# Kernel tuning notes

Measured on AMD Instinct MI355X. Metric: run time of the kernel, lower is better.

Reference implementation:

```python
import jax, jax.numpy as jnp
import numpy as np

B, T, N_EMBD, HEAD = 8, 2048, 1024, 64


def setup_inputs() -> dict:
    key = jax.random.key(0)
    kx, kq, kk, kv = jax.random.split(key, 4)
    s = 1.0 / np.sqrt(N_EMBD)
    return {
        "x": jax.random.normal(kx, (B, T, N_EMBD), dtype=jnp.float32),
        "Wq": jax.random.normal(kq, (N_EMBD, HEAD), dtype=jnp.float32) * s,
        "Wk": jax.random.normal(kk, (N_EMBD, HEAD), dtype=jnp.float32) * s,
        "Wv": jax.random.normal(kv, (N_EMBD, HEAD), dtype=jnp.float32) * s,
    }


def reference(x, Wq, Wk, Wv):
    # x: [B, T, C] with C = n_embd
    Bs, Ts, C = x.shape
    q = jnp.einsum('btc,ch->bth', x, Wq)  # [B,T,H]
    k = jnp.einsum('btc,ch->bth', x, Wk)
    v = jnp.einsum('btc,ch->bth', x, Wv)
    # NOTE: original scales by C**-0.5 where C = n_embd (input dim), not head_size
    scale = jnp.asarray(C, x.dtype) ** -0.5
    wei = jnp.einsum('bth,bsh->bts', q, k) * scale  # [B,T,T]
    causal = jnp.tril(jnp.ones((Ts, Ts), dtype=bool))
    wei = jnp.where(causal, wei, jnp.asarray(-jnp.inf, wei.dtype))
    wei = jax.nn.softmax(wei, axis=-1)
    out = jnp.einsum('bts,bsh->bth', wei, v)  # [B,T,H]
    return out
```

## Files before the change

kernel.cpp:

```cpp
#include <hip/hip_runtime.h>
#include <hip/hip_bf16.h>
#include <math.h>

#define B_ 8
#define T_ 2048
#define C_ 1024
#define H_ 64

typedef __attribute__((ext_vector_type(8))) __bf16 bf16x8;
typedef __attribute__((ext_vector_type(4))) float f32x4;

static __device__ inline unsigned short f2bf_u(float f) {
    __bf16 b = (__bf16)f;
    return __builtin_bit_cast(unsigned short, b);
}
static __device__ inline unsigned int pack2(float lo, float hi) {
    return (unsigned int)f2bf_u(lo) | ((unsigned int)f2bf_u(hi) << 16);
}

__global__ void prep_w_kernel(const float* __restrict__ Wq,
                              const float* __restrict__ Wk,
                              const float* __restrict__ Wv,
                              unsigned short* __restrict__ Wp) {
    int idx = blockIdx.x * 256 + threadIdx.x;
    if (idx >= C_ * 192) return;
    int k = idx / 192;
    int n = idx % 192;
    const float* W = (n < 64) ? Wq : (n < 128) ? Wk : Wv;
    float val = W[k * 64 + (n & 63)];
    Wp[((size_t)(k >> 5) * 192 + n) * 32 + (k & 31)] = f2bf_u(val);
}

__global__ __launch_bounds__(256, 3) void proj_kernel(
        const float* __restrict__ x, const unsigned short* __restrict__ Wp,
        unsigned short* __restrict__ q, unsigned short* __restrict__ k,
        unsigned short* __restrict__ vT) {
    __shared__ f32x4 red[4][12][64];
    const int wave = threadIdx.x >> 6;
    const int lane = threadIdx.x & 63;
    const int col  = lane & 15;
    const int quad = lane >> 4;
    const int row0 = blockIdx.x * 16;
    const float* xrow = x + (size_t)(row0 + col) * C_ + quad * 8;

    f32x4 acc[12];
    #pragma unroll
    for (int i = 0; i < 12; i++) acc[i] = (f32x4){0.f, 0.f, 0.f, 0.f};

    const int kt0 = wave * 8;
    #pragma unroll 4
    for (int kt = kt0; kt < kt0 + 8; kt++) {
        const float4* xp = (const float4*)(xrow + kt * 32);
        float4 x0 = xp[0];
        float4 x1 = xp[1];
        bf16x8 a;
        a[0] = (__bf16)x0.x; a[1] = (__bf16)x0.y; a[2] = (__bf16)x0.z; a[3] = (__bf16)x0.w;
        a[4] = (__bf16)x1.x; a[5] = (__bf16)x1.y; a[6] = (__bf16)x1.z; a[7] = (__bf16)x1.w;
        const unsigned short* wb = Wp + ((size_t)kt * 192 + col) * 32 + quad * 8;
        #pragma unroll
        for (int n = 0; n < 12; n++) {
            bf16x8 bfrag = *(const bf16x8*)(wb + n * (16 * 32));
            acc[n] = __builtin_amdgcn_mfma_f32_16x16x32_bf16(a, bfrag, acc[n], 0, 0, 0);
        }
    }
    #pragma unroll
    for (int n = 0; n < 12; n++) red[wave][n][lane] = acc[n];
    __syncthreads();

    const int bi   = row0 >> 11;
    const int trow = row0 & 2047;
    #pragma unroll
    for (int j = 0; j < 3; j++) {
        int n = wave * 3 + j;
        f32x4 s = red[0][n][lane];
        s += red[1][n][lane];
        s += red[2][n][lane];
        s += red[3][n][lane];
        if (n < 8) {
            unsigned short* dst = (n < 4) ? q : k;
            int cc = (n & 3) * 16 + col;
            #pragma unroll
            for (int r = 0; r < 4; r++) {
                int grow = row0 + quad * 4 + r;
                dst[(size_t)grow * 64 + cc] = f2bf_u(s[r]);
            }
        } else {
            int hh = (n - 8) * 16 + col;
            ushort4 pk;
            pk.x = f2bf_u(s[0]); pk.y = f2bf_u(s[1]);
            pk.z = f2bf_u(s[2]); pk.w = f2bf_u(s[3]);
            *(ushort4*)(vT + ((size_t)bi * 64 + hh) * T_ + trow + quad * 4) = pk;
        }
    }
}

__global__ __launch_bounds__(256, 4) void attn_kernel(
        const unsigned short* __restrict__ q, const unsigned short* __restrict__ k,
        const unsigned short* __restrict__ vT, float* __restrict__ out) {
    __shared__ unsigned int tbuf[4][2][16 * 20];
    __shared__ float so[4][16][68];
    __shared__ float sl[4][16];
    const int wave = threadIdx.x >> 6;
    const int lane = threadIdx.x & 63;
    const int col  = lane & 15;
    const int quad = lane >> 4;
    const int bi = blockIdx.x & 7;
    const int ti = 127 - (blockIdx.x >> 3);
    const int t0 = ti * 16;
    const unsigned short* qb = q  + (size_t)bi * T_ * 64;
    const unsigned short* kb = k  + (size_t)bi * T_ * 64;
    const unsigned short* vb = vT + (size_t)bi * 64 * T_;

    bf16x8 qf0 = *(const bf16x8*)(qb + (size_t)(t0 + col) * 64 + quad * 8);
    bf16x8 qf1 = *(const bf16x8*)(qb + (size_t)(t0 + col) * 64 + 32 + quad * 8);

    f32x4 o[4];
    #pragma unroll
    for (int i = 0; i < 4; i++) o[i] = (f32x4){0.f, 0.f, 0.f, 0.f};
    float lacc = 0.f;
    const float cs = 0.03125f * 1.44269504088896f;
    const int qrow = t0 + col;

    const int nit = (t0 + 47) >> 5;
    const int ci  = (nit + 3) >> 2;
    const int it0 = wave * ci;
    const int it1 = min(it0 + ci, nit);

    for (int it = it0; it < it1; ++it) {
        const int s0 = it * 32;
        bf16x8 kf00 = *(const bf16x8*)(kb + (size_t)(s0 + col) * 64 + quad * 8);
        bf16x8 kf01 = *(const bf16x8*)(kb + (size_t)(s0 + col) * 64 + 32 + quad * 8);
        bf16x8 kf10 = *(const bf16x8*)(kb + (size_t)(s0 + 16 + col) * 64 + quad * 8);
        bf16x8 kf11 = *(const bf16x8*)(kb + (size_t)(s0 + 16 + col) * 64 + 32 + quad * 8);
        f32x4 sa = (f32x4){0.f, 0.f, 0.f, 0.f};
        f32x4 sb = (f32x4){0.f, 0.f, 0.f, 0.f};
        sa = __builtin_amdgcn_mfma_f32_16x16x32_bf16(kf00, qf0, sa, 0, 0, 0);
        sa = __builtin_amdgcn_mfma_f32_16x16x32_bf16(kf01, qf1, sa, 0, 0, 0);
        sb = __builtin_amdgcn_mfma_f32_16x16x32_bf16(kf10, qf0, sb, 0, 0, 0);
        sb = __builtin_amdgcn_mfma_f32_16x16x32_bf16(kf11, qf1, sb, 0, 0, 0);

        float pa[4], pb[4];
        #pragma unroll
        for (int r = 0; r < 4; r++) {
            int ka = s0 + quad * 4 + r;
            pa[r] = (ka      <= qrow) ? exp2f(sa[r] * cs) : 0.f;
            pb[r] = (ka + 16 <= qrow) ? exp2f(sb[r] * cs) : 0.f;
            lacc += pa[r] + pb[r];
        }
        unsigned int* tb = &tbuf[wave][it & 1][0];
        *(uint2*)&tb[col * 20 + 2 * quad] =
            make_uint2(pack2(pa[0], pa[1]), pack2(pa[2], pa[3]));
        *(uint2*)&tb[col * 20 + 8 + 2 * quad] =
            make_uint2(pack2(pb[0], pb[1]), pack2(pb[2], pb[3]));
        bf16x8 pf = *(const bf16x8*)&tb[col * 20 + 4 * quad];
        #pragma unroll
        for (int ht = 0; ht < 4; ht++) {
            bf16x8 vf = *(const bf16x8*)(vb + (size_t)(ht * 16 + col) * T_ + s0 + quad * 8);
            o[ht] = __builtin_amdgcn_mfma_f32_16x16x32_bf16(vf, pf, o[ht], 0, 0, 0);
        }
    }

    lacc += __shfl_xor(lacc, 16);
    lacc += __shfl_xor(lacc, 32);
    if (quad == 0) sl[wave][col] = lacc;
    #pragma unroll
    for (int ht = 0; ht < 4; ht++)
        *(f32x4*)&so[wave][col][ht * 16 + quad * 4] = o[ht];
    __syncthreads();

    for (int e = threadIdx.x; e < 1024; e += 256) {
        int qq = e >> 6, h = e & 63;
        float L = sl[0][qq] + sl[1][qq] + sl[2][qq] + sl[3][qq];
        float val = so[0][qq][h] + so[1][qq][h] + so[2][qq][h] + so[3][qq][h];
        out[((size_t)bi * T_ + t0 + qq) * 64 + h] = val / L;
    }
}

extern "C" void kernel_launch(void* const* d_in, const int* in_sizes, int n_in,
                              void* d_out, int out_size, void* d_ws, size_t ws_size,
                              hipStream_t stream) {
    const float* x  = (const float*)d_in[0];
    const float* Wq = (const float*)d_in[1];
    const float* Wk = (const float*)d_in[2];
    const float* Wv = (const float*)d_in[3];
    float* out = (float*)d_out;

    unsigned short* Wp  = (unsigned short*)d_ws;
    unsigned short* qws = (unsigned short*)((char*)d_ws + 0x60000);
    unsigned short* kws = (unsigned short*)((char*)d_ws + 0x60000 + 0x200000);
    unsigned short* vws = (unsigned short*)((char*)d_ws + 0x60000 + 0x400000);

    prep_w_kernel<<<(C_ * 192 + 255) / 256, 256, 0, stream>>>(Wq, Wk, Wv, Wp);
    proj_kernel<<<(B_ * T_) / 16, 256, 0, stream>>>(x, Wp, qws, kws, vws);
    attn_kernel<<<(B_ * T_) / 16, 256, 0, stream>>>(qws, kws, vws, out);
}
```

Before: 160.3 us.

## Restructure projection kernel to stage weight slice in LDS and split outputs across blocks

The projection kernel now launches 192 blocks of 512 threads. Each block takes one 64-column slice of the packed weights (Q, K or V) and loads all of it into shared memory with global_load_lds. Each wave then computes a full-K 32x64 output tile, so the cross-wave reduction through shared memory goes away. In exchange, x is read three times (once per projection group), and only 192 blocks are launched, which may underfill the GPU.

```diff
diff --git a/kernel.cpp b/kernel.cpp
--- a/kernel.cpp
+++ b/kernel.cpp
@@ -31,65 +31,89 @@
     Wp[((size_t)(k >> 5) * 192 + n) * 32 + (k & 31)] = f2bf_u(val);
 }
 
-__global__ __launch_bounds__(256, 3) void proj_kernel(
+__global__ __launch_bounds__(512) void proj_kernel(
         const float* __restrict__ x, const unsigned short* __restrict__ Wp,
         unsigned short* __restrict__ q, unsigned short* __restrict__ k,
         unsigned short* __restrict__ vT) {
-    __shared__ f32x4 red[4][12][64];
+    __shared__ unsigned short wlds[32][64][32];
     const int wave = threadIdx.x >> 6;
     const int lane = threadIdx.x & 63;
     const int col  = lane & 15;
     const int quad = lane >> 4;
-    const int row0 = blockIdx.x * 16;
-    const float* xrow = x + (size_t)(row0 + col) * C_ + quad * 8;
-
-    f32x4 acc[12];
-    #pragma unroll
-    for (int i = 0; i < 12; i++) acc[i] = (f32x4){0.f, 0.f, 0.f, 0.f};
-
-    const int kt0 = wave * 8;
+    const int g     = blockIdx.x % 3;
+    const int chunk = blockIdx.x / 3;
+    const int n0 = g * 64;
+
+    #pragma unroll
+    for (int i = 0; i < 4; i++) {
+        int kt = wave * 4 + i;
+        #pragma unroll
+        for (int part = 0; part < 4; part++) {
+            const unsigned short* src =
+                Wp + ((size_t)kt * 192 + n0 + part * 16) * 32 + lane * 8;
+            __builtin_amdgcn_global_load_lds(
+                (const __attribute__((address_space(1))) unsigned int*)src,
+                (__attribute__((address_space(3))) unsigned int*)&wlds[kt][part * 16][0],
+                16, 0, 0);
+        }
+    }
+    __syncthreads();
+
+    const int r0 = chunk * 256 + wave * 32;
+    const float* xb0 = x + (size_t)(r0 + col) * C_;
+    const float* xb1 = x + (size_t)(r0 + 16 + col) * C_;
+
+    f32x4 acc[8];
+    #pragma unroll
+    for (int i = 0; i < 8; i++) acc[i] = (f32x4){0.f, 0.f, 0.f, 0.f};
+
     #pragma unroll 4
-    for (int kt = kt0; kt < kt0 + 8; kt++) {
-        const float4* xp = (const float4*)(xrow + kt * 32);
-        float4 x0 = xp[0];
-        float4 x1 = xp[1];
-        bf16x8 a;
-        a[0] = (__bf16)x0.x; a[1] = (__bf16)x0.y; a[2] = (__bf16)x0.z; a[3] = (__bf16)x0.w;
-        a[4] = (__bf16)x1.x; a[5] = (__bf16)x1.y; a[6] = (__bf16)x1.z; a[7] = (__bf16)x1.w;
-        const unsigned short* wb = Wp + ((size_t)kt * 192 + col) * 32 + quad * 8;
-        #pragma unroll
-        for (int n = 0; n < 12; n++) {
-            bf16x8 bfrag = *(const bf16x8*)(wb + n * (16 * 32));
-            acc[n] = __builtin_amdgcn_mfma_f32_16x16x32_bf16(a, bfrag, acc[n], 0, 0, 0);
-        }
-    }
-    #pragma unroll
-    for (int n = 0; n < 12; n++) red[wave][n][lane] = acc[n];
-    __syncthreads();
-
-    const int bi   = row0 >> 11;
-    const int trow = row0 & 2047;
-    #pragma unroll
-    for (int j = 0; j < 3; j++) {
-        int n = wave * 3 + j;
-        f32x4 s = red[0][n][lane];
-        s += red[1][n][lane];
-        s += red[2][n][lane];
-        s += red[3][n][lane];
-        if (n < 8) {
-            unsigned short* dst = (n < 4) ? q : k;
-            int cc = (n & 3) * 16 + col;
+    for (int kt = 0; kt < 32; kt++) {
+        const float4* xq0 = (const float4*)(xb0 + kt * 32 + quad * 8);
+        const float4* xq1 = (const float4*)(xb1 + kt * 32 + quad * 8);
+        float4 p00 = xq0[0], p01 = xq0[1];
+        float4 p10 = xq1[0], p11 = xq1[1];
+        bf16x8 a0, a1;
+        a0[0] = (__bf16)p00.x; a0[1] = (__bf16)p00.y; a0[2] = (__bf16)p00.z; a0[3] = (__bf16)p00.w;
+        a0[4] = (__bf16)p01.x; a0[5] = (__bf16)p01.y; a0[6] = (__bf16)p01.z; a0[7] = (__bf16)p01.w;
+        a1[0] = (__bf16)p10.x; a1[1] = (__bf16)p10.y; a1[2] = (__bf16)p10.z; a1[3] = (__bf16)p10.w;
+        a1[4] = (__bf16)p11.x; a1[5] = (__bf16)p11.y; a1[6] = (__bf16)p11.z; a1[7] = (__bf16)p11.w;
+        #pragma unroll
+        for (int nt = 0; nt < 4; nt++) {
+            bf16x8 b = *(const bf16x8*)&wlds[kt][nt * 16 + col][quad * 8];
+            acc[nt]     = __builtin_amdgcn_mfma_f32_16x16x32_bf16(a0, b, acc[nt], 0, 0, 0);
+            acc[4 + nt] = __builtin_amdgcn_mfma_f32_16x16x32_bf16(a1, b, acc[4 + nt], 0, 0, 0);
+        }
+    }
+
+    if (g < 2) {
+        unsigned short* dst = (g == 0) ? q : k;
+        #pragma unroll
+        for (int mt = 0; mt < 2; mt++) {
             #pragma unroll
-            for (int r = 0; r < 4; r++) {
-                int grow = row0 + quad * 4 + r;
-                dst[(size_t)grow * 64 + cc] = f2bf_u(s[r]);
+            for (int nt = 0; nt < 4; nt++) {
+                f32x4 s = acc[mt * 4 + nt];
+                int cc = nt * 16 + col;
+                int grow = r0 + mt * 16 + quad * 4;
+                #pragma unroll
+                for (int r = 0; r < 4; r++)
+                    dst[(size_t)(grow + r) * 64 + cc] = f2bf_u(s[r]);
             }
-        } else {
-            int hh = (n - 8) * 16 + col;
-            ushort4 pk;
-            pk.x = f2bf_u(s[0]); pk.y = f2bf_u(s[1]);
-            pk.z = f2bf_u(s[2]); pk.w = f2bf_u(s[3]);
-            *(ushort4*)(vT + ((size_t)bi * 64 + hh) * T_ + trow + quad * 4) = pk;
+        }
+    } else {
+        #pragma unroll
+        for (int mt = 0; mt < 2; mt++) {
+            #pragma unroll
+            for (int nt = 0; nt < 4; nt++) {
+                f32x4 s = acc[mt * 4 + nt];
+                int hh = nt * 16 + col;
+                int row = r0 + mt * 16 + quad * 4;
+                int bi = row >> 11, trow = row & 2047;
+                ushort4 pk;
+                pk.x = f2bf_u(s[0]); pk.y = f2bf_u(s[1]);
+                pk.z = f2bf_u(s[2]); pk.w = f2bf_u(s[3]);
+                *(ushort4*)(vT + ((size_t)bi * 64 + hh) * T_ + trow) = pk;
+            }
         }
     }
 }
@@ -191,6 +215,6 @@
     unsigned short* vws = (unsigned short*)((char*)d_ws + 0x60000 + 0x400000);
 
     prep_w_kernel<<<(C_ * 192 + 255) / 256, 256, 0, stream>>>(Wq, Wk, Wv, Wp);
-    proj_kernel<<<(B_ * T_) / 16, 256, 0, stream>>>(x, Wp, qws, kws, vws);
+    proj_kernel<<<64 * 3, 512, 0, stream>>>(x, Wp, qws, kws, vws);
     attn_kernel<<<(B_ * T_) / 16, 256, 0, stream>>>(qws, kws, vws, out);
 }
```

Measured after the change: 171.5 us. 7.0% more time.

## Split projection N across waves with shared-memory x staging and prefetch

Applied to the files above, without the earlier changes.

The projection kernel no longer splits the K dimension across waves with a shared-memory reduction. Each wave now owns 48 output columns and walks the full K range. The x tile is converted to bf16 once into a triple-buffered shared buffer, with loads rotated among the waves, and W fragments are software-prefetched one step ahead. This removes the cross-wave reduction and the fourfold redundant x loading and conversion, and raises occupancy to 4 blocks per SM. In exchange it adds a __syncthreads on each of the 32 K steps and makes the K loop serial per wave.

```diff
diff --git a/kernel.cpp b/kernel.cpp
--- a/kernel.cpp
+++ b/kernel.cpp
@@ -31,65 +31,89 @@
     Wp[((size_t)(k >> 5) * 192 + n) * 32 + (k & 31)] = f2bf_u(val);
 }
 
-__global__ __launch_bounds__(256, 3) void proj_kernel(
+#define XPAD 40
+__global__ __launch_bounds__(256, 4) void proj_kernel(
         const float* __restrict__ x, const unsigned short* __restrict__ Wp,
         unsigned short* __restrict__ q, unsigned short* __restrict__ k,
         unsigned short* __restrict__ vT) {
-    __shared__ f32x4 red[4][12][64];
+    __shared__ unsigned short xbf[3][16][XPAD];
     const int wave = threadIdx.x >> 6;
     const int lane = threadIdx.x & 63;
     const int col  = lane & 15;
     const int quad = lane >> 4;
     const int row0 = blockIdx.x * 16;
-    const float* xrow = x + (size_t)(row0 + col) * C_ + quad * 8;
-
-    f32x4 acc[12];
-    #pragma unroll
-    for (int i = 0; i < 12; i++) acc[i] = (f32x4){0.f, 0.f, 0.f, 0.f};
-
-    const int kt0 = wave * 8;
-    #pragma unroll 4
-    for (int kt = kt0; kt < kt0 + 8; kt++) {
-        const float4* xp = (const float4*)(xrow + kt * 32);
-        float4 x0 = xp[0];
-        float4 x1 = xp[1];
-        bf16x8 a;
-        a[0] = (__bf16)x0.x; a[1] = (__bf16)x0.y; a[2] = (__bf16)x0.z; a[3] = (__bf16)x0.w;
-        a[4] = (__bf16)x1.x; a[5] = (__bf16)x1.y; a[6] = (__bf16)x1.z; a[7] = (__bf16)x1.w;
-        const unsigned short* wb = Wp + ((size_t)kt * 192 + col) * 32 + quad * 8;
-        #pragma unroll
-        for (int n = 0; n < 12; n++) {
-            bf16x8 bfrag = *(const bf16x8*)(wb + n * (16 * 32));
-            acc[n] = __builtin_amdgcn_mfma_f32_16x16x32_bf16(a, bfrag, acc[n], 0, 0, 0);
-        }
-    }
-    #pragma unroll
-    for (int n = 0; n < 12; n++) red[wave][n][lane] = acc[n];
+    const int n0   = wave * 48;
+
+    const int srow = lane >> 2;
+    const int scol = (lane & 3) * 8;
+    const float* sbase = x + (size_t)(row0 + srow) * C_ + scol;
+
+    f32x4 acc[3];
+    #pragma unroll
+    for (int i = 0; i < 3; i++) acc[i] = (f32x4){0.f, 0.f, 0.f, 0.f};
+
+    if (wave < 2) {
+        const float4* p = (const float4*)(sbase + wave * 32);
+        float4 u0 = p[0], u1 = p[1];
+        bf16x8 w;
+        w[0] = (__bf16)u0.x; w[1] = (__bf16)u0.y; w[2] = (__bf16)u0.z; w[3] = (__bf16)u0.w;
+        w[4] = (__bf16)u1.x; w[5] = (__bf16)u1.y; w[6] = (__bf16)u1.z; w[7] = (__bf16)u1.w;
+        *(bf16x8*)&xbf[wave][srow][scol] = w;
+    }
+    const unsigned short* wb = Wp + (size_t)(n0 + col) * 32 + quad * 8;
+    bf16x8 bcur0 = *(const bf16x8*)(wb);
+    bf16x8 bcur1 = *(const bf16x8*)(wb + 16 * 32);
+    bf16x8 bcur2 = *(const bf16x8*)(wb + 32 * 32);
     __syncthreads();
 
-    const int bi   = row0 >> 11;
-    const int trow = row0 & 2047;
-    #pragma unroll
-    for (int j = 0; j < 3; j++) {
-        int n = wave * 3 + j;
-        f32x4 s = red[0][n][lane];
-        s += red[1][n][lane];
-        s += red[2][n][lane];
-        s += red[3][n][lane];
-        if (n < 8) {
-            unsigned short* dst = (n < 4) ? q : k;
-            int cc = (n & 3) * 16 + col;
+    #pragma unroll 2
+    for (int kt = 0; kt < 32; kt++) {
+        const bool own = (kt + 2 < 32) && (((kt + 2) & 3) == wave);
+        float4 u0, u1;
+        if (own) {
+            const float4* p = (const float4*)(sbase + (kt + 2) * 32);
+            u0 = p[0]; u1 = p[1];
+        }
+        bf16x8 bn0, bn1, bn2;
+        if (kt + 1 < 32) {
+            const unsigned short* wn = wb + (size_t)(kt + 1) * 192 * 32;
+            bn0 = *(const bf16x8*)(wn);
+            bn1 = *(const bf16x8*)(wn + 16 * 32);
+            bn2 = *(const bf16x8*)(wn + 32 * 32);
+        }
+        bf16x8 a = *(const bf16x8*)&xbf[kt % 3][col][quad * 8];
+        acc[0] = __builtin_amdgcn_mfma_f32_16x16x32_bf16(a, bcur0, acc[0], 0, 0, 0);
+        acc[1] = __builtin_amdgcn_mfma_f32_16x16x32_bf16(a, bcur1, acc[1], 0, 0, 0);
+        acc[2] = __builtin_amdgcn_mfma_f32_16x16x32_bf16(a, bcur2, acc[2], 0, 0, 0);
+        bcur0 = bn0; bcur1 = bn1; bcur2 = bn2;
+        if (own) {
+            bf16x8 w;
+            w[0] = (__bf16)u0.x; w[1] = (__bf16)u0.y; w[2] = (__bf16)u0.z; w[3] = (__bf16)u0.w;
+            w[4] = (__bf16)u1.x; w[5] = (__bf16)u1.y; w[6] = (__bf16)u1.z; w[7] = (__bf16)u1.w;
+            *(bf16x8*)&xbf[(kt + 2) % 3][srow][scol] = w;
+        }
+        __syncthreads();
+    }
+
+    #pragma unroll
+    for (int nt = 0; nt < 3; nt++) {
+        f32x4 s = acc[nt];
+        int c = n0 + nt * 16;
+        int g = c >> 6;
+        if (g < 2) {
+            unsigned short* dst = (g == 0) ? q : k;
+            int cc = (c & 63) + col;
+            int grow = row0 + quad * 4;
             #pragma unroll
-            for (int r = 0; r < 4; r++) {
-                int grow = row0 + quad * 4 + r;
-                dst[(size_t)grow * 64 + cc] = f2bf_u(s[r]);
-            }
+            for (int r = 0; r < 4; r++)
+                dst[(size_t)(grow + r) * 64 + cc] = f2bf_u(s[r]);
         } else {
-            int hh = (n - 8) * 16 + col;
+            int hh = (c - 128) + col;
+            int bi = row0 >> 11, trow = (row0 & 2047) + quad * 4;
             ushort4 pk;
             pk.x = f2bf_u(s[0]); pk.y = f2bf_u(s[1]);
             pk.z = f2bf_u(s[2]); pk.w = f2bf_u(s[3]);
-            *(ushort4*)(vT + ((size_t)bi * 64 + hh) * T_ + trow + quad * 4) = pk;
+            *(ushort4*)(vT + ((size_t)bi * 64 + hh) * T_ + trow) = pk;
         }
     }
 }
```

Result: no change. 161.9 us (+1.0%).
